# Kernel tuning notes

Measured on AMD Instinct MI355X. Metric: run time of the kernel, lower is better.

## Reference

```python
import jax, jax.numpy as jnp
import numpy as np

NUM_CODES = 4096
EMBED_DIM = 256
N_TOKENS = 65536
COMMITMENT_COST = 0.1


def setup_inputs() -> dict:
    key = jax.random.key(0)
    k1, k2 = jax.random.split(key)
    z_e = jax.random.normal(k1, (N_TOKENS, EMBED_DIM), dtype=jnp.float32)
    embeddings = jax.random.normal(k2, (NUM_CODES, EMBED_DIM), dtype=jnp.float32)
    return {"z_e": z_e, "embeddings": embeddings}


def reference(z_e, embeddings):
    # Squared Euclidean distances (argmin-equivalent to torch.cdist):
    # d2[n,k] = |z_n|^2 - 2 z_n.E_k + |E_k|^2
    z_sq = jnp.sum(z_e * z_e, axis=-1, keepdims=True)          # [N,1]
    e_sq = jnp.sum(embeddings * embeddings, axis=-1)            # [K]
    d2 = z_sq - 2.0 * (z_e @ embeddings.T) + e_sq[None, :]      # [N,K]
    indices = jnp.argmin(d2, axis=-1)                           # [N] int

    z_q = embeddings[indices]                                   # [N,D] gather

    # commitment loss: mse(detach(z_q), z_e)
    diff = jax.lax.stop_gradient(z_q) - z_e
    commitment_loss = COMMITMENT_COST * jnp.mean(diff * diff)

    # straight-through estimator
    z_q_st = z_e + jax.lax.stop_gradient(z_q - z_e)

    # perplexity from code usage histogram (avoids materializing one-hot)
    counts = jnp.zeros((NUM_CODES,), dtype=jnp.float32).at[indices].add(1.0)
    avg_probs = counts / z_e.shape[0]
    perplexity = jnp.exp(-jnp.sum(avg_probs * jnp.log(avg_probs + 1e-10)))

    return z_q_st, indices, commitment_loss, perplexity
```

## Files before the change

kernel.cpp:

```cpp
#include <hip/hip_runtime.h>

#define N_TOKENS   65536
#define NUM_CODES  4096
#define EMBED_DIM  256

#define IDX_OFF  ((size_t)N_TOKENS * EMBED_DIM)
#define LOSS_OFF (IDX_OFF + N_TOKENS)

#define DELTA 0.2f
#define UCAP  16384
#define RT    8

typedef _Float16 half8 __attribute__((ext_vector_type(8)));
typedef float    f32x4 __attribute__((ext_vector_type(4)));
typedef unsigned long long u64;

__device__ __forceinline__ void gl_lds16(const void* g, void* l) {
    __builtin_amdgcn_global_load_lds(
        (const __attribute__((address_space(1))) unsigned int*)g,
        (__attribute__((address_space(3))) unsigned int*)l, 16, 0, 0);
}

__global__ void k_convE(const float* __restrict__ E, _Float16* __restrict__ Eh) {
    int gid = blockIdx.x * 256 + threadIdx.x;
    int n  = gid >> 5;
    int kg = gid & 31;
    const float* src = E + (size_t)n * EMBED_DIM + kg * 8;
    float4 a = *(const float4*)src;
    float4 b = *(const float4*)(src + 4);
    int ct = n >> 4, l15 = n & 15, kc = kg >> 2, q = kg & 3;
    int lane = q * 16 + l15;
    half8 hv;
    hv[0]=(_Float16)a.x; hv[1]=(_Float16)a.y; hv[2]=(_Float16)a.z; hv[3]=(_Float16)a.w;
    hv[4]=(_Float16)b.x; hv[5]=(_Float16)b.y; hv[6]=(_Float16)b.z; hv[7]=(_Float16)b.w;
    *(half8*)(Eh + ((size_t)(ct * 8 + kc) * 64 + lane) * 8) = hv;
}

__global__ void k_esq(const float* __restrict__ E, float* __restrict__ esq) {
    int k = blockIdx.x;
    int l = threadIdx.x;
    float4 v = *(const float4*)(E + (size_t)k * EMBED_DIM + l * 4);
    float s = v.x * v.x + v.y * v.y + v.z * v.z + v.w * v.w;
    #pragma unroll
    for (int off = 32; off; off >>= 1) s += __shfl_down(s, off, 64);
    if (l == 0) esq[k] = s;
}

__global__ void k_transpose(const float* __restrict__ E, float* __restrict__ Et) {
    __shared__ float t[32][33];
    int tx = threadIdx.x & 31, ty = threadIdx.x >> 5;
    int c0 = blockIdx.x * 32, d0 = blockIdx.y * 32;
    #pragma unroll
    for (int i = 0; i < 4; ++i)
        t[ty + 8 * i][tx] = E[(size_t)(c0 + ty + 8 * i) * EMBED_DIM + d0 + tx];
    __syncthreads();
    #pragma unroll
    for (int i = 0; i < 4; ++i)
        Et[(size_t)(d0 + ty + 8 * i) * NUM_CODES + c0 + tx] = t[tx][ty + 8 * i];
}

__global__ __launch_bounds__(256) __attribute__((amdgpu_waves_per_eu(2, 2)))
void k_argmin_mfma(const float* __restrict__ Z, const _Float16* __restrict__ Eh,
                   const float* __restrict__ esq, int* __restrict__ out_idx,
                   int* __restrict__ ulist, int* __restrict__ ucount) {
    __shared__ __align__(16) _Float16 Bs[2][16384];
    __shared__ float esq_s[NUM_CODES];

    const int tid  = threadIdx.x;
    const int lane = tid & 63;
    const int w    = tid >> 6;
    const int l15  = lane & 15;
    const int q    = lane >> 4;
    const int tb   = blockIdx.x;

#define STAGE(itn, bb) do {                                                        \
        const _Float16* _src = Eh + ((size_t)(itn) << 14) + (w * 8) * 512 + lane * 8; \
        _Float16* _dst = &Bs[bb][(w * 8) * 512];                                   \
        _Pragma("unroll")                                                          \
        for (int s = 0; s < 8; ++s)                                                \
            gl_lds16(_src + s * 512, _dst + s * 512);                              \
    } while (0)

    STAGE(0, 0);
    STAGE(1, 1);

    for (int i = tid; i < NUM_CODES; i += 256) esq_s[i] = esq[i];

    half8 A[2][8];
    const float* Zb = Z + ((size_t)tb * 128 + w * 32) * EMBED_DIM;
    #pragma unroll
    for (int rt = 0; rt < 2; ++rt) {
        const float* Zr = Zb + (rt * 16 + l15) * EMBED_DIM + q * 8;
        #pragma unroll
        for (int kc = 0; kc < 8; ++kc) {
            float4 a = *(const float4*)(Zr + kc * 32);
            float4 b = *(const float4*)(Zr + kc * 32 + 4);
            half8 hv;
            hv[0]=(_Float16)a.x; hv[1]=(_Float16)a.y; hv[2]=(_Float16)a.z; hv[3]=(_Float16)a.w;
            hv[4]=(_Float16)b.x; hv[5]=(_Float16)b.y; hv[6]=(_Float16)b.z; hv[7]=(_Float16)b.w;
            A[rt][kc] = hv;
        }
    }

    float best[8], sec[8];
    int   bidx[8];
    #pragma unroll
    for (int k = 0; k < 8; ++k) { best[k] = 1e30f; sec[k] = 1e30f; bidx[k] = 0; }

    __syncthreads();

    for (int it = 0; it < NUM_CODES / 64; ++it) {
        const int b = it & 1;

        if (it == NUM_CODES / 64 - 1) asm volatile("s_waitcnt vmcnt(0)" ::: "memory");
        else                          asm volatile("s_waitcnt vmcnt(8)" ::: "memory");
        asm volatile("s_barrier" ::: "memory");

        f32x4 acc[2][4];
        #pragma unroll
        for (int rt = 0; rt < 2; ++rt)
            #pragma unroll
            for (int ct = 0; ct < 4; ++ct) acc[rt][ct] = (f32x4)0.0f;

        __builtin_amdgcn_s_setprio(1);
        #pragma unroll
        for (int kc = 0; kc < 8; ++kc) {
            half8 bf[4];
            #pragma unroll
            for (int ct = 0; ct < 4; ++ct)
                bf[ct] = *(const half8*)(&Bs[b][(ct * 8 + kc) * 512 + lane * 8]);
            #pragma unroll
            for (int rt = 0; rt < 2; ++rt)
                #pragma unroll
                for (int ct = 0; ct < 4; ++ct)
                    acc[rt][ct] = __builtin_amdgcn_mfma_f32_16x16x32_f16(A[rt][kc], bf[ct], acc[rt][ct], 0, 0, 0);
        }
        __builtin_amdgcn_s_setprio(0);

        const int code_base = it * 64 + l15;
        float e0 = esq_s[code_base];
        float e1 = esq_s[code_base + 16];
        float e2 = esq_s[code_base + 32];
        float e3 = esq_s[code_base + 48];
        #pragma unroll
        for (int rt = 0; rt < 2; ++rt)
            #pragma unroll
            for (int r = 0; r < 4; ++r) {
                int k = rt * 4 + r;
                float v0 = fmaf(-2.0f, acc[rt][0][r], e0);
                float v1 = fmaf(-2.0f, acc[rt][1][r], e1);
                float v2 = fmaf(-2.0f, acc[rt][2][r], e2);
                float v3 = fmaf(-2.0f, acc[rt][3][r], e3);
                bool t01 = v1 < v0;
                float w01 = t01 ? v1 : v0, l01 = t01 ? v0 : v1;
                int   i01 = code_base + (t01 ? 16 : 0);
                bool t23 = v3 < v2;
                float w23 = t23 ? v3 : v2, l23 = t23 ? v2 : v3;
                int   i23 = code_base + 32 + (t23 ? 16 : 0);
                bool tf = w23 < w01;
                float wv = tf ? w23 : w01;
                int   wi = tf ? i23 : i01;
                float rsec = fminf(fminf(fmaxf(w01, w23), l01), l23);
                float ob = best[k];
                bool tb_ = wv < ob;
                sec[k]  = fminf(fminf(sec[k], rsec), fmaxf(ob, wv));
                best[k] = tb_ ? wv : ob;
                bidx[k] = tb_ ? wi : bidx[k];
            }

        asm volatile("s_barrier" ::: "memory");
        if (it + 2 < NUM_CODES / 64) STAGE(it + 2, b);
    }
#undef STAGE

    #pragma unroll
    for (int m = 1; m <= 8; m <<= 1) {
        #pragma unroll
        for (int k = 0; k < 8; ++k) {
            float ob = __shfl_xor(best[k], m, 64);
            float os = __shfl_xor(sec[k],  m, 64);
            int   oi = __shfl_xor(bidx[k], m, 64);
            float ns = fminf(fminf(sec[k], os), fmaxf(best[k], ob));
            bool t = (ob < best[k]) || (ob == best[k] && oi < bidx[k]);
            best[k] = t ? ob : best[k];
            bidx[k] = t ? oi : bidx[k];
            sec[k]  = ns;
        }
    }

    if (l15 == 0) {
        #pragma unroll
        for (int k = 0; k < 8; ++k) {
            int row   = w * 32 + (k >> 2) * 16 + q * 4 + (k & 3);
            int token = tb * 128 + row;
            out_idx[token] = bidx[k];
            if (sec[k] - best[k] < DELTA) {
                int p = atomicAdd(ucount, 1);
                if (p < UCAP) ulist[p] = token;
            }
        }
    }
}

__launch_bounds__(256)
__global__ void k_refine(const float* __restrict__ Z, const float* __restrict__ Et,
                         const float* __restrict__ esq, const int* __restrict__ ulist,
                         const int* __restrict__ ucount, u64* __restrict__ umin) {
    int cnt = *ucount; if (cnt > UCAP) cnt = UCAP;
    const int g   = blockIdx.x >> 2;
    const int qtr = blockIdx.x & 3;
    if (g * RT >= cnt) return;

    __shared__ float zs[RT][256];
    const int tid  = threadIdx.x;
    const int lane = tid & 63;

    #pragma unroll
    for (int t = 0; t < RT; ++t) {
        int u = g * RT + t;
        int tok = ulist[(u < cnt) ? u : g * RT];
        zs[t][tid] = Z[(size_t)tok * EMBED_DIM + tid];
    }
    __syncthreads();

    const int c0 = qtr * 1024 + tid * 4;
    f32x4 acc[RT];
    #pragma unroll
    for (int t = 0; t < RT; ++t) acc[t] = (f32x4)0.0f;

    for (int d4 = 0; d4 < 64; ++d4) {
        f32x4 e0 = *(const f32x4*)(Et + (size_t)(d4 * 4 + 0) * NUM_CODES + c0);
        f32x4 e1 = *(const f32x4*)(Et + (size_t)(d4 * 4 + 1) * NUM_CODES + c0);
        f32x4 e2 = *(const f32x4*)(Et + (size_t)(d4 * 4 + 2) * NUM_CODES + c0);
        f32x4 e3 = *(const f32x4*)(Et + (size_t)(d4 * 4 + 3) * NUM_CODES + c0);
        #pragma unroll
        for (int t = 0; t < RT; ++t) {
            f32x4 z4 = *(const f32x4*)&zs[t][d4 * 4];
            acc[t] += z4.x * e0;
            acc[t] += z4.y * e1;
            acc[t] += z4.z * e2;
            acc[t] += z4.w * e3;
        }
    }

    f32x4 eq = *(const f32x4*)(esq + c0);
    #pragma unroll
    for (int t = 0; t < RT; ++t) {
        u64 p = ~0ull;
        #pragma unroll
        for (int r = 0; r < 4; ++r) {
            float v = fmaf(-2.0f, acc[t][r], eq[r]) + 4096.0f;
            u64 cand = ((u64)__float_as_uint(v) << 32) | (unsigned)(c0 + r);
            p = cand < p ? cand : p;
        }
        #pragma unroll
        for (int m = 1; m <= 32; m <<= 1) {
            u64 o = __shfl_xor(p, m, 64);
            p = o < p ? o : p;
        }
        int u = g * RT + t;
        if (lane == 0 && u < cnt) atomicMin(umin + u, p);
    }
}

__global__ void k_rwrite(const int* __restrict__ ulist, const int* __restrict__ ucount,
                         const u64* __restrict__ umin, int* __restrict__ out_idx) {
    int cnt = *ucount; if (cnt > UCAP) cnt = UCAP;
    int u = blockIdx.x * 256 + threadIdx.x;
    if (u < cnt) out_idx[ulist[u]] = (int)(umin[u] & 0xFFFFFFFFu);
}

__global__ void k_gather(const float* __restrict__ Z, const float* __restrict__ E,
                         float* __restrict__ out,
                         float* __restrict__ loss_parts, unsigned* __restrict__ hist) {
    int wave = threadIdx.x >> 6, lane = threadIdx.x & 63;
    int token = blockIdx.x * 4 + wave;
    int* idxi = (int*)(out + IDX_OFF);
    int k = idxi[token];
    float4 z = *(const float4*)(Z + (size_t)token * EMBED_DIM + lane * 4);
    float4 qv = *(const float4*)(E + (size_t)k * EMBED_DIM + lane * 4);
    *(float4*)(out + (size_t)token * EMBED_DIM + lane * 4) = qv;
    float dx = qv.x - z.x, dy = qv.y - z.y, dz = qv.z - z.z, dw = qv.w - z.w;
    float s = dx * dx + dy * dy + dz * dz + dw * dw;
    #pragma unroll
    for (int off = 32; off; off >>= 1) s += __shfl_down(s, off, 64);
    if (lane == 0) {
        atomicAdd(loss_parts + (blockIdx.x & 1023), s);
        atomicAdd(hist + k, 1u);
        out[IDX_OFF + token] = (float)k;
    }
}

__global__ void k_final(const float* __restrict__ loss_parts,
                        const unsigned* __restrict__ hist, float* __restrict__ out) {
    __shared__ float red[256];
    int t = threadIdx.x;
    float s = 0.0f;
    for (int i = t; i < 1024; i += 256) s += loss_parts[i];
    red[t] = s;
    __syncthreads();
    #pragma unroll
    for (int off = 128; off; off >>= 1) {
        if (t < off) red[t] += red[t + off];
        __syncthreads();
    }
    float loss = 0.1f * red[0] / (float)(N_TOKENS * EMBED_DIM);

    float h = 0.0f;
    for (int i = t; i < NUM_CODES; i += 256) {
        float p = (float)hist[i] / (float)N_TOKENS;
        h += p * logf(p + 1e-10f);
    }
    __syncthreads();
    red[t] = h;
    __syncthreads();
    #pragma unroll
    for (int off = 128; off; off >>= 1) {
        if (t < off) red[t] += red[t + off];
        __syncthreads();
    }
    if (t == 0) {
        out[LOSS_OFF]     = loss;
        out[LOSS_OFF + 1] = expf(-red[0]);
    }
}

extern "C" void kernel_launch(void* const* d_in, const int* in_sizes, int n_in,
                              void* d_out, int out_size, void* d_ws, size_t ws_size,
                              hipStream_t stream) {
    const float* Z = (const float*)d_in[0];
    const float* E = (const float*)d_in[1];
    float* out = (float*)d_out;
    char*  ob  = (char*)d_out;
    char*  ws  = (char*)d_ws;

    _Float16* Eh   = (_Float16*)(ob + 50331648);
    float*    Et   = (float*)(ob + 54525952);
    u64*      umin = (u64*)(ob + 58720256);
    int*      idx  = (int*)(out + IDX_OFF);

    float*    esq        = (float*)ws;
    int*      ulist      = (int*)(ws + 16384);
    int*      ucount     = (int*)(ws + 81920);
    float*    loss_parts = (float*)(ws + 81984);
    unsigned* hist       = (unsigned*)(ws + 86080);

    hipMemsetAsync(ws + 81920, 0, 64 + 4096 + 16384, stream);
    hipMemsetAsync(umin, 0xFF, (size_t)UCAP * 8, stream);

    k_convE      <<<(NUM_CODES * 32) / 256, 256, 0, stream>>>(E, Eh);
    k_esq        <<<NUM_CODES, 64, 0, stream>>>(E, esq);
    k_transpose  <<<dim3(NUM_CODES / 32, EMBED_DIM / 32), 256, 0, stream>>>(E, Et);
    k_argmin_mfma<<<N_TOKENS / 128, 256, 0, stream>>>(Z, Eh, esq, idx, ulist, ucount);
    k_refine     <<<4 * (UCAP / RT), 256, 0, stream>>>(Z, Et, esq, ulist, ucount, umin);
    k_rwrite     <<<UCAP / 256, 256, 0, stream>>>(ulist, ucount, umin, idx);
    k_gather     <<<N_TOKENS / 4, 256, 0, stream>>>(Z, E, out, loss_parts, hist);
    k_final      <<<1, 256, 0, stream>>>(loss_parts, hist, out);
}
```

Before: 350.0 us.

## Split argmin block over 8 waves sharing 128-code tiles with LDS merge

The argmin kernel now runs 512 threads per block. Each pair of waves shares the same 32 token rows and takes one half of a 128-code tile, so every LDS stage brings in twice as many codes and the loop runs half as many iterations. Per-wave best and second-best values are merged through LDS before the index is written and ambiguous tokens are flagged. The barrier and next-stage prefetch are moved ahead of the distance epilogue so loads overlap the compare work. LDS use doubles to about 144KB, which limits each CU to one block, and the waves_per_eu hint is removed.

```diff
diff --git a/kernel.cpp b/kernel.cpp
--- a/kernel.cpp
+++ b/kernel.cpp
@@ -59,22 +59,24 @@
         Et[(size_t)(d0 + ty + 8 * i) * NUM_CODES + c0 + tx] = t[tx][ty + 8 * i];
 }
 
-__global__ __launch_bounds__(256) __attribute__((amdgpu_waves_per_eu(2, 2)))
+__global__ __launch_bounds__(512)
 void k_argmin_mfma(const float* __restrict__ Z, const _Float16* __restrict__ Eh,
                    const float* __restrict__ esq, int* __restrict__ out_idx,
                    int* __restrict__ ulist, int* __restrict__ ucount) {
-    __shared__ __align__(16) _Float16 Bs[2][16384];
+    __shared__ __align__(16) _Float16 Bs[2][32768];
     __shared__ float esq_s[NUM_CODES];
 
     const int tid  = threadIdx.x;
     const int lane = tid & 63;
     const int w    = tid >> 6;
+    const int wt   = w >> 1;
+    const int wc   = w & 1;
     const int l15  = lane & 15;
     const int q    = lane >> 4;
     const int tb   = blockIdx.x;
 
 #define STAGE(itn, bb) do {                                                        \
-        const _Float16* _src = Eh + ((size_t)(itn) << 14) + (w * 8) * 512 + lane * 8; \
+        const _Float16* _src = Eh + ((size_t)(itn) << 15) + (w * 8) * 512 + lane * 8; \
         _Float16* _dst = &Bs[bb][(w * 8) * 512];                                   \
         _Pragma("unroll")                                                          \
         for (int s = 0; s < 8; ++s)                                                \
@@ -84,10 +86,10 @@
     STAGE(0, 0);
     STAGE(1, 1);
 
-    for (int i = tid; i < NUM_CODES; i += 256) esq_s[i] = esq[i];
+    for (int i = tid; i < NUM_CODES; i += 512) esq_s[i] = esq[i];
 
     half8 A[2][8];
-    const float* Zb = Z + ((size_t)tb * 128 + w * 32) * EMBED_DIM;
+    const float* Zb = Z + ((size_t)tb * 128 + wt * 32) * EMBED_DIM;
     #pragma unroll
     for (int rt = 0; rt < 2; ++rt) {
         const float* Zr = Zb + (rt * 16 + l15) * EMBED_DIM + q * 8;
@@ -109,35 +111,39 @@
 
     __syncthreads();
 
-    for (int it = 0; it < NUM_CODES / 64; ++it) {
+    const int NIT = NUM_CODES / 128;
+    for (int it = 0; it < NIT; ++it) {
         const int b = it & 1;
 
-        if (it == NUM_CODES / 64 - 1) asm volatile("s_waitcnt vmcnt(0)" ::: "memory");
-        else                          asm volatile("s_waitcnt vmcnt(8)" ::: "memory");
+        if (it == NIT - 1) asm volatile("s_waitcnt vmcnt(0)" ::: "memory");
+        else               asm volatile("s_waitcnt vmcnt(8)" ::: "memory");
         asm volatile("s_barrier" ::: "memory");
 
         f32x4 acc[2][4];
         #pragma unroll
         for (int rt = 0; rt < 2; ++rt)
             #pragma unroll
-            for (int ct = 0; ct < 4; ++ct) acc[rt][ct] = (f32x4)0.0f;
+            for (int c = 0; c < 4; ++c) acc[rt][c] = (f32x4)0.0f;
 
         __builtin_amdgcn_s_setprio(1);
         #pragma unroll
         for (int kc = 0; kc < 8; ++kc) {
             half8 bf[4];
             #pragma unroll
-            for (int ct = 0; ct < 4; ++ct)
-                bf[ct] = *(const half8*)(&Bs[b][(ct * 8 + kc) * 512 + lane * 8]);
+            for (int c = 0; c < 4; ++c)
+                bf[c] = *(const half8*)(&Bs[b][((wc * 4 + c) * 8 + kc) * 512 + lane * 8]);
             #pragma unroll
             for (int rt = 0; rt < 2; ++rt)
                 #pragma unroll
-                for (int ct = 0; ct < 4; ++ct)
-                    acc[rt][ct] = __builtin_amdgcn_mfma_f32_16x16x32_f16(A[rt][kc], bf[ct], acc[rt][ct], 0, 0, 0);
+                for (int c = 0; c < 4; ++c)
+                    acc[rt][c] = __builtin_amdgcn_mfma_f32_16x16x32_f16(A[rt][kc], bf[c], acc[rt][c], 0, 0, 0);
         }
         __builtin_amdgcn_s_setprio(0);
 
-        const int code_base = it * 64 + l15;
+        asm volatile("s_barrier" ::: "memory");
+        if (it + 2 < NIT) STAGE(it + 2, b);
+
+        const int code_base = it * 128 + wc * 64 + l15;
         float e0 = esq_s[code_base];
         float e1 = esq_s[code_base + 16];
         float e2 = esq_s[code_base + 32];
@@ -167,9 +173,6 @@
                 best[k] = tb_ ? wv : ob;
                 bidx[k] = tb_ ? wi : bidx[k];
             }
-
-        asm volatile("s_barrier" ::: "memory");
-        if (it + 2 < NUM_CODES / 64) STAGE(it + 2, b);
     }
 #undef STAGE
 
@@ -188,16 +191,33 @@
         }
     }
 
+    __syncthreads();
+    float* mb = (float*)Bs;
+    float* ms = mb + 256;
+    int*   mi = (int*)(mb + 512);
     if (l15 == 0) {
         #pragma unroll
         for (int k = 0; k < 8; ++k) {
-            int row   = w * 32 + (k >> 2) * 16 + q * 4 + (k & 3);
-            int token = tb * 128 + row;
-            out_idx[token] = bidx[k];
-            if (sec[k] - best[k] < DELTA) {
-                int p = atomicAdd(ucount, 1);
-                if (p < UCAP) ulist[p] = token;
-            }
+            int row = wt * 32 + (k >> 2) * 16 + q * 4 + (k & 3);
+            mb[row * 2 + wc] = best[k];
+            ms[row * 2 + wc] = sec[k];
+            mi[row * 2 + wc] = bidx[k];
+        }
+    }
+    __syncthreads();
+    if (tid < 128) {
+        float b0 = mb[tid * 2], b1 = mb[tid * 2 + 1];
+        float s0 = ms[tid * 2], s1 = ms[tid * 2 + 1];
+        int   i0 = mi[tid * 2], i1 = mi[tid * 2 + 1];
+        bool t = (b1 < b0) || (b1 == b0 && i1 < i0);
+        float bb = t ? b1 : b0;
+        int   ii = t ? i1 : i0;
+        float ss = fminf(fminf(s0, s1), fmaxf(b0, b1));
+        int token = tb * 128 + tid;
+        out_idx[token] = ii;
+        if (ss - bb < DELTA) {
+            int p = atomicAdd(ucount, 1);
+            if (p < UCAP) ulist[p] = token;
         }
     }
 }
@@ -351,7 +371,7 @@
     k_convE      <<<(NUM_CODES * 32) / 256, 256, 0, stream>>>(E, Eh);
     k_esq        <<<NUM_CODES, 64, 0, stream>>>(E, esq);
     k_transpose  <<<dim3(NUM_CODES / 32, EMBED_DIM / 32), 256, 0, stream>>>(E, Et);
-    k_argmin_mfma<<<N_TOKENS / 128, 256, 0, stream>>>(Z, Eh, esq, idx, ulist, ucount);
+    k_argmin_mfma<<<N_TOKENS / 128, 512, 0, stream>>>(Z, Eh, esq, idx, ulist, ucount);
     k_refine     <<<4 * (UCAP / RT), 256, 0, stream>>>(Z, Et, esq, ulist, ucount, umin);
     k_rwrite     <<<UCAP / 256, 256, 0, stream>>>(ulist, ucount, umin, idx);
     k_gather     <<<N_TOKENS / 4, 256, 0, stream>>>(Z, E, out, loss_parts, hist);
```

Result: slower. 375.2 us (+7.2%).
